# Optimization experiments

Hardware: AMD Instinct MI355X
Metric: run time of the kernel (lower is better)

## Reference

```python
import jax, jax.numpy as jnp
import numpy as np
from jax import lax

B, C, H, W = 4, 256, 64, 64
NH, DK, DV = 8, 32, 32
KER, PAD = 3, 1


def conv1x1(x, w, b=None):
    # x: [B,C,H,W], w: [O,C] (1x1 conv kernel), b: [O] or None
    y = jnp.einsum('bchw,oc->bohw', x, w)
    if b is not None:
        y = y + b[None, :, None, None]
    return y


def unfold(x, k, pad):
    # F.unfold equivalent: [B,C,H,W] -> [B, C*k*k, H, W] (channel-major patch order)
    return lax.conv_general_dilated_patches(x, (k, k), (1, 1), [(pad, pad), (pad, pad)])


def local_attention(q, k, v, kernel, pad, n_head):
    # per-head local windowed attention over a kernel x kernel neighborhood
    b, c, h, w = q.shape
    d = c // n_head
    kk = kernel * kernel
    qh = q.reshape(b, n_head, d, h, w)
    kpat = unfold(k, kernel, pad).reshape(b, n_head, d, kk, h, w)
    vpat = unfold(v, kernel, pad).reshape(b, n_head, d, kk, h, w)
    scale = 1.0 / np.sqrt(float(d)).astype(np.float32)
    logits = jnp.einsum('bhdxy,bhdkxy->bhkxy', qh, kpat) * scale
    attn = jax.nn.softmax(logits, axis=2)
    out = jnp.einsum('bhkxy,bhdkxy->bhdxy', attn, vpat)
    return out.reshape(b, c, h, w)


def layernorm2d(x, g, b, eps=1e-6):
    mu = jnp.mean(x, axis=1, keepdims=True)
    var = jnp.mean((x - mu) ** 2, axis=1, keepdims=True)
    return (x - mu) / jnp.sqrt(var + eps) * g[None, :, None, None] + b[None, :, None, None]


def batchnorm2d(x, g, b, eps=1e-5):
    mu = jnp.mean(x, axis=(0, 2, 3), keepdims=True)
    var = jnp.mean((x - mu) ** 2, axis=(0, 2, 3), keepdims=True)
    return (x - mu) / jnp.sqrt(var + eps) * g[None, :, None, None] + b[None, :, None, None]


def mha(xq, xkv, wq, wk, wv, wfc, g, bias, kernel, pad):
    residual = xq
    q = conv1x1(xq, wq)
    k = conv1x1(xkv, wk)
    v = conv1x1(xkv, wv)
    o = local_attention(q, k, v, kernel, pad, NH)
    o = conv1x1(o, wfc) + residual
    return layernorm2d(o, g, bias)


def ffn(x, w1, b1, w2, b2, g, bias):
    residual = x
    y = conv1x1(jax.nn.relu(conv1x1(x, w1, b1)), w2, b2)
    y = batchnorm2d(y, g, bias)
    return y + residual


def setup_inputs() -> dict:
    key = jax.random.key(0)
    ks = jax.random.split(key, 16)
    s = 0.05
    d = {
        'input1': jax.random.normal(ks[0], (B, C, H, W), jnp.float32),
        'input2': jax.random.normal(ks[1], (B, C, H, W), jnp.float32),
        'slf_wq': jax.random.normal(ks[2], (NH * DK, C), jnp.float32) * s,
        'slf_wk': jax.random.normal(ks[3], (NH * DK, C), jnp.float32) * s,
        'slf_wv': jax.random.normal(ks[4], (NH * DV, C), jnp.float32) * s,
        'slf_fc': jax.random.normal(ks[5], (C, NH * DV), jnp.float32) * s,
        'slf_g': jnp.ones((C,), jnp.float32),
        'slf_b': jnp.zeros((C,), jnp.float32),
        'crs_wq': jax.random.normal(ks[6], (NH * DK, C), jnp.float32) * s,
        'crs_wk': jax.random.normal(ks[7], (NH * DK, C), jnp.float32) * s,
        'crs_wv': jax.random.normal(ks[8], (NH * DV, C), jnp.float32) * s,
        'crs_fc': jax.random.normal(ks[9], (C, NH * DV), jnp.float32) * s,
        'crs_g': jnp.ones((C,), jnp.float32),
        'crs_b': jnp.zeros((C,), jnp.float32),
        'ffn_w1': jax.random.normal(ks[10], (C, C), jnp.float32) * s,
        'ffn_b1': jnp.zeros((C,), jnp.float32),
        'ffn_w2': jax.random.normal(ks[11], (C, C), jnp.float32) * s,
        'ffn_b2': jnp.zeros((C,), jnp.float32),
        'ffn_bn_g': jnp.ones((C,), jnp.float32),
        'ffn_bn_b': jnp.zeros((C,), jnp.float32),
        'kernel': KER,
        'pad': PAD,
    }
    return d


def reference(input1, input2, slf_wq, slf_wk, slf_wv, slf_fc, slf_g, slf_b,
              crs_wq, crs_wk, crs_wv, crs_fc, crs_g, crs_b,
              ffn_w1, ffn_b1, ffn_w2, ffn_b2, ffn_bn_g, ffn_bn_b, kernel, pad):
    slf1 = mha(input1, input1, slf_wq, slf_wk, slf_wv, slf_fc, slf_g, slf_b, kernel, pad)
    slf2 = mha(input2, input2, slf_wq, slf_wk, slf_wv, slf_fc, slf_g, slf_b, kernel, pad)
    crs1 = mha(slf1, slf2, crs_wq, crs_wk, crs_wv, crs_fc, crs_g, crs_b, kernel, pad)
    crs2 = mha(slf2, slf1, crs_wq, crs_wk, crs_wv, crs_fc, crs_g, crs_b, kernel, pad)
    out1 = ffn(crs1, ffn_w1, ffn_b1, ffn_w2, ffn_b2, ffn_bn_g, ffn_bn_b)
    out2 = ffn(crs2, ffn_w1, ffn_b1, ffn_w2, ffn_b2, ffn_bn_g, ffn_bn_b)
    return (out1, out2)
```

## Files before the change

### kernel.cpp

```cpp
#include <hip/hip_runtime.h>
#include <stdint.h>

using u16 = unsigned short;
typedef __bf16 bf16x8 __attribute__((ext_vector_type(8)));
typedef float f32x4 __attribute__((ext_vector_type(4)));

#define NPIX 16384
#define CDIM 256

__device__ __forceinline__ float b2f(u16 u) {
  union { unsigned i; float f; } c; c.i = ((unsigned)u) << 16; return c.f;
}
__device__ __forceinline__ u16 f2b(float x) {
  union { float f; unsigned i; } c; c.f = x;
  unsigned r = c.i + 0x7fffu + ((c.i >> 16) & 1u);
  return (u16)(r >> 16);
}
__device__ __forceinline__ unsigned pack2(float a, float b) {
  return (unsigned)f2b(a) | ((unsigned)f2b(b) << 16);
}
__device__ __forceinline__ void unpack8(uint4 w, float* f) {
  f[0] = b2f((u16)(w.x & 0xffffu)); f[1] = b2f((u16)(w.x >> 16));
  f[2] = b2f((u16)(w.y & 0xffffu)); f[3] = b2f((u16)(w.y >> 16));
  f[4] = b2f((u16)(w.z & 0xffffu)); f[5] = b2f((u16)(w.z >> 16));
  f[6] = b2f((u16)(w.w & 0xffffu)); f[7] = b2f((u16)(w.w >> 16));
}

__device__ __forceinline__ void async16(u16* l, const u16* g) {
  __builtin_amdgcn_global_load_lds((const __attribute__((address_space(1))) void*)g,
                                   (__attribute__((address_space(3))) void*)l, 16, 0, 0);
}

template <int NI>
__device__ __forceinline__ void stage_swz(u16* lds, const u16* src, int tid) {
#pragma unroll
  for (int i = 0; i < NI; ++i) {
    const int idx = i * 256 + tid;
    const int row = idx >> 3;
    const int c8 = (idx & 7) ^ (row & 7);
    async16(lds + idx * 8, src + (size_t)row * 256 + c8 * 8);
  }
}

__global__ void cvt_w(const float* s0, const float* s1, const float* s2,
                      const float* s3, const float* s4, const float* s5,
                      const float* s6, const float* s7, const float* s8,
                      const float* s9, u16* __restrict__ dst,
                      float* __restrict__ stats) {
  if (blockIdx.x == 0 && blockIdx.y == 0) {
    ((float4*)stats)[threadIdx.x] = float4{0.f, 0.f, 0.f, 0.f};
  }
  const int m = blockIdx.y;
  const float* s;
  switch (m) {
    case 0: s = s0; break; case 1: s = s1; break; case 2: s = s2; break;
    case 3: s = s3; break; case 4: s = s4; break; case 5: s = s5; break;
    case 6: s = s6; break; case 7: s = s7; break; case 8: s = s8; break;
    default: s = s9; break;
  }
  const int i = (blockIdx.x * 256 + threadIdx.x) * 4;
  float4 v = *(const float4*)(s + i);
  uint2 o;
  o.x = pack2(v.x, v.y);
  o.y = pack2(v.z, v.w);
  *(uint2*)(dst + (size_t)m * 65536 + i) = o;
}

__global__ void transpose_in(const float* __restrict__ x1, const float* __restrict__ x2,
                             u16* __restrict__ X1, u16* __restrict__ X2) {
  __shared__ u16 tile[64][65];
  const int t = threadIdx.x;
  const int z = blockIdx.z;
  const float* x = (z < 4) ? x1 : x2;
  u16* X = (z < 4) ? X1 : X2;
  const int b = z & 3, c0 = blockIdx.y * 64, hw0 = blockIdx.x * 64;
  {
    const int hw_l = t & 63, cb = t >> 6;
#pragma unroll
    for (int i = 0; i < 16; ++i) {
      const int c_l = cb * 16 + i;
      tile[c_l][hw_l] = f2b(x[((size_t)(b * 256 + c0 + c_l)) * 4096 + hw0 + hw_l]);
    }
  }
  __syncthreads();
  {
    const int c_l = t & 63, hb = t >> 6;
#pragma unroll
    for (int i = 0; i < 16; ++i) {
      const int hw_l = hb * 16 + i;
      X[((size_t)(b * 4096 + hw0 + hw_l)) * 256 + c0 + c_l] = tile[c_l][hw_l];
    }
  }
}

struct P6 { const u16* X[6]; const u16* W[3]; u16* D[6]; };

__global__ void gemm_qkv(P6 a) {
  __shared__ u16 As[128 * 64];
  __shared__ u16 Bs[128 * 64];
  const int tid = threadIdx.x;
  const int wave = tid >> 6, lane = tid & 63;
  const int p0 = blockIdx.x * 128;
  const int g = blockIdx.y >> 1, o0 = (blockIdx.y & 1) * 128;
  const int z = blockIdx.z;
  const u16* X = a.X[z * 3 + g];
  const u16* W = a.W[g];
  u16* D = a.D[z * 3 + g];
  const int wr = wave & 1, wc = wave >> 1;
  const int l15 = lane & 15, l4 = lane >> 4;
  const int sw = l15 & 7;
  f32x4 acc[4][4] = {};

  for (int kt = 0; kt < 4; ++kt) {
    const int k0 = kt * 64;
    stage_swz<4>(As, X + (size_t)p0 * 256 + k0, tid);
    stage_swz<4>(Bs, W + (size_t)o0 * 256 + k0, tid);
    __syncthreads();
#pragma unroll
    for (int kk = 0; kk < 2; ++kk) {
      const int cs = ((kk * 4 + l4) ^ sw) * 8;
      bf16x8 af[4], bfr[4];
#pragma unroll
      for (int mi = 0; mi < 4; ++mi)
        af[mi] = *(const bf16x8*)&As[(wr * 64 + mi * 16 + l15) * 64 + cs];
#pragma unroll
      for (int ni = 0; ni < 4; ++ni)
        bfr[ni] = *(const bf16x8*)&Bs[(wc * 64 + ni * 16 + l15) * 64 + cs];
#pragma unroll
      for (int mi = 0; mi < 4; ++mi)
#pragma unroll
        for (int ni = 0; ni < 4; ++ni)
          acc[mi][ni] = __builtin_amdgcn_mfma_f32_16x16x32_bf16(af[mi], bfr[ni],
                                                                acc[mi][ni], 0, 0, 0);
    }
    __syncthreads();
  }
#pragma unroll
  for (int ni = 0; ni < 4; ++ni) {
    const int o = o0 + wc * 64 + ni * 16 + l15;
#pragma unroll
    for (int mi = 0; mi < 4; ++mi)
#pragma unroll
      for (int r = 0; r < 4; ++r) {
        const int p = p0 + wr * 64 + mi * 16 + l4 * 4 + r;
        D[(size_t)p * 256 + o] = f2b(acc[mi][ni][r]);
      }
  }
}

struct Pfc { const u16* X[2]; const u16* res[2]; u16* dst[2];
             const u16* W; const float* g; const float* b; };

__global__ void gemm_fc_ln(Pfc a) {
  __shared__ u16 As[64 * 64];
  __shared__ u16 Bs[256 * 64];
  __shared__ float red[2][64][4];
  const int tid = threadIdx.x;
  const int wave = tid >> 6, lane = tid & 63;
  const int l15 = lane & 15, l4 = lane >> 4;
  const int sw = l15 & 7;
  const int p0 = blockIdx.x * 64;
  const int z = blockIdx.y;
  const u16* X = a.X[z];
  const u16* res = a.res[z];
  u16* dst = a.dst[z];
  f32x4 acc[4][4] = {};

  for (int kt = 0; kt < 4; ++kt) {
    const int k0 = kt * 64;
    stage_swz<2>(As, X + (size_t)p0 * 256 + k0, tid);
    stage_swz<8>(Bs, a.W + k0, tid);
    __syncthreads();
#pragma unroll
    for (int kk = 0; kk < 2; ++kk) {
      const int cs = ((kk * 4 + l4) ^ sw) * 8;
      bf16x8 af[4], bfr[4];
#pragma unroll
      for (int mi = 0; mi < 4; ++mi)
        af[mi] = *(const bf16x8*)&As[(mi * 16 + l15) * 64 + cs];
#pragma unroll
      for (int ni = 0; ni < 4; ++ni)
        bfr[ni] = *(const bf16x8*)&Bs[(wave * 64 + ni * 16 + l15) * 64 + cs];
#pragma unroll
      for (int mi = 0; mi < 4; ++mi)
#pragma unroll
        for (int ni = 0; ni < 4; ++ni)
          acc[mi][ni] = __builtin_amdgcn_mfma_f32_16x16x32_bf16(af[mi], bfr[ni],
                                                                acc[mi][ni], 0, 0, 0);
    }
    __syncthreads();
  }

#pragma unroll
  for (int mi = 0; mi < 4; ++mi) {
#pragma unroll
    for (int r = 0; r < 4; ++r) {
      const int pl = mi * 16 + l4 * 4 + r;
      const int p = p0 + pl;
      float s = 0.f, s2 = 0.f;
#pragma unroll
      for (int ni = 0; ni < 4; ++ni) {
        const int o = wave * 64 + ni * 16 + l15;
        float vv = acc[mi][ni][r] + b2f(res[(size_t)p * 256 + o]);
        acc[mi][ni][r] = vv;
        s += vv; s2 += vv * vv;
      }
#pragma unroll
      for (int m = 1; m < 16; m <<= 1) {
        s += __shfl_xor(s, m); s2 += __shfl_xor(s2, m);
      }
      if (l15 == 0) { red[0][pl][wave] = s; red[1][pl][wave] = s2; }
    }
  }
  __syncthreads();

  float gv[4], bv[4];
#pragma unroll
  for (int ni = 0; ni < 4; ++ni) {
    const int o = wave * 64 + ni * 16 + l15;
    gv[ni] = a.g[o]; bv[ni] = a.b[o];
  }
#pragma unroll
  for (int mi = 0; mi < 4; ++mi) {
#pragma unroll
    for (int r = 0; r < 4; ++r) {
      const int pl = mi * 16 + l4 * 4 + r;
      const float st = red[0][pl][0] + red[0][pl][1] + red[0][pl][2] + red[0][pl][3];
      const float s2t = red[1][pl][0] + red[1][pl][1] + red[1][pl][2] + red[1][pl][3];
      const float mu = st * (1.f / 256.f);
      const float var = s2t * (1.f / 256.f) - mu * mu;
      const float inv = rsqrtf(var + 1e-6f);
      const int p = p0 + pl;
#pragma unroll
      for (int ni = 0; ni < 4; ++ni) {
        const int o = wave * 64 + ni * 16 + l15;
        dst[(size_t)p * 256 + o] = f2b((acc[mi][ni][r] - mu) * inv * gv[ni] + bv[ni]);
      }
    }
  }
}

struct Pg { const u16* X[2]; u16* Y[2]; float* st[2];
            const u16* W; const float* bias; };

template <int HAS_BIAS, int RELU, int DO_STATS>
__global__ void gemm_kernel(Pg a) {
  __shared__ u16 As[128 * 64];
  __shared__ u16 Bs[64 * 64];
  const int tid = threadIdx.x;
  const int wave = tid >> 6, lane = tid & 63;
  const int p0 = blockIdx.x * 128, o0 = blockIdx.y * 64;
  const int z = blockIdx.z;
  const u16* X = a.X[z];
  u16* Y = a.Y[z];
  float* st = a.st[z];
  const int wr = wave & 1, wc = wave >> 1;
  const int l15 = lane & 15, l4 = lane >> 4;
  const int sw = l15 & 7;
  f32x4 acc[4][2] = {};

  for (int kt = 0; kt < 4; ++kt) {
    const int k0 = kt * 64;
    stage_swz<4>(As, X + (size_t)p0 * 256 + k0, tid);
    stage_swz<2>(Bs, a.W + (size_t)o0 * 256 + k0, tid);
    __syncthreads();
#pragma unroll
    for (int kk = 0; kk < 2; ++kk) {
      const int cs = ((kk * 4 + l4) ^ sw) * 8;
      bf16x8 af[4], bfr[2];
#pragma unroll
      for (int mi = 0; mi < 4; ++mi)
        af[mi] = *(const bf16x8*)&As[(wr * 64 + mi * 16 + l15) * 64 + cs];
#pragma unroll
      for (int ni = 0; ni < 2; ++ni)
        bfr[ni] = *(const bf16x8*)&Bs[(wc * 32 + ni * 16 + l15) * 64 + cs];
#pragma unroll
      for (int mi = 0; mi < 4; ++mi)
#pragma unroll
        for (int ni = 0; ni < 2; ++ni)
          acc[mi][ni] = __builtin_amdgcn_mfma_f32_16x16x32_bf16(af[mi], bfr[ni],
                                                                acc[mi][ni], 0, 0, 0);
    }
    __syncthreads();
  }
#pragma unroll
  for (int ni = 0; ni < 2; ++ni) {
    const int o = o0 + wc * 32 + ni * 16 + l15;
    float bvv = 0.f;
    if (HAS_BIAS) bvv = a.bias[o];
    float s = 0.f, s2 = 0.f;
#pragma unroll
    for (int mi = 0; mi < 4; ++mi) {
#pragma unroll
      for (int r = 0; r < 4; ++r) {
        const int p = p0 + wr * 64 + mi * 16 + l4 * 4 + r;
        float v = acc[mi][ni][r] + bvv;
        if (RELU) v = fmaxf(v, 0.f);
        const u16 hv = f2b(v);
        Y[(size_t)p * 256 + o] = hv;
        if (DO_STATS) { const float vr = b2f(hv); s += vr; s2 += vr * vr; }
      }
    }
    if (DO_STATS) {
      s += __shfl_xor(s, 16); s2 += __shfl_xor(s2, 16);
      s += __shfl_xor(s, 32); s2 += __shfl_xor(s2, 32);
      if (l4 == 0) { atomicAdd(&st[o], s); atomicAdd(&st[256 + o], s2); }
    }
  }
}

struct Pat { const u16* Q[2]; const u16* K[2]; const u16* V[2]; u16* O[2]; };

__global__ void attn_kernel(Pat a) {
  const int s = blockIdx.y;
  const u16* __restrict__ Q = a.Q[s];
  const u16* __restrict__ K = a.K[s];
  const u16* __restrict__ V = a.V[s];
  u16* O = a.O[s];
  const int t = blockIdx.x * 256 + threadIdx.x;
  const int p = t >> 3, h = t & 7;
  const int y = (p >> 6) & 63, x = p & 63;
  const size_t base = (size_t)p * 256 + h * 32;

  float q[32];
  {
    const uint4* qp = (const uint4*)(Q + base);
#pragma unroll
    for (int i = 0; i < 4; ++i) { uint4 w = qp[i]; unpack8(w, q + i * 8); }
  }
  float lg[9];
  float mx = -1e30f;
#pragma unroll
  for (int j = 0; j < 9; ++j) {
    const int dy = j / 3 - 1, dx = j % 3 - 1;
    const int ny = y + dy, nx = x + dx;
    float l = 0.f;
    if ((unsigned)ny < 64u && (unsigned)nx < 64u) {
      const uint4* kp = (const uint4*)(K + base + (ptrdiff_t)(dy * 64 + dx) * 256);
      float acc = 0.f;
#pragma unroll
      for (int i = 0; i < 4; ++i) {
        float kf[8]; unpack8(kp[i], kf);
#pragma unroll
        for (int d = 0; d < 8; ++d) acc += q[i * 8 + d] * kf[d];
      }
      l = acc * 0.17677669529663687f;
    }
    lg[j] = l;
    mx = fmaxf(mx, l);
  }
  float pr[9], den = 0.f;
#pragma unroll
  for (int j = 0; j < 9; ++j) { pr[j] = __expf(lg[j] - mx); den += pr[j]; }
  float out[32];
#pragma unroll
  for (int d = 0; d < 32; ++d) out[d] = 0.f;
#pragma unroll
  for (int j = 0; j < 9; ++j) {
    const int dy = j / 3 - 1, dx = j % 3 - 1;
    const int ny = y + dy, nx = x + dx;
    if ((unsigned)ny < 64u && (unsigned)nx < 64u) {
      const uint4* vp = (const uint4*)(V + base + (ptrdiff_t)(dy * 64 + dx) * 256);
      const float w = pr[j];
#pragma unroll
      for (int i = 0; i < 4; ++i) {
        float vf[8]; unpack8(vp[i], vf);
#pragma unroll
        for (int d = 0; d < 8; ++d) out[i * 8 + d] += w * vf[d];
      }
    }
  }
  const float inv = 1.f / den;
  uint4* op = (uint4*)(O + base);
#pragma unroll
  for (int i = 0; i < 4; ++i) {
    uint4 w;
    w.x = pack2(out[i * 8 + 0] * inv, out[i * 8 + 1] * inv);
    w.y = pack2(out[i * 8 + 2] * inv, out[i * 8 + 3] * inv);
    w.z = pack2(out[i * 8 + 4] * inv, out[i * 8 + 5] * inv);
    w.w = pack2(out[i * 8 + 6] * inv, out[i * 8 + 7] * inv);
    op[i] = w;
  }
}

struct Pbn { const u16* U[2]; const u16* res[2]; const float* st[2];
             float* out[2]; const float* g; const float* b; };

__global__ void bn_apply(Pbn a) {
  __shared__ float tile[64][65];
  const int t = threadIdx.x;
  const int s = blockIdx.z >> 2, b = blockIdx.z & 3;
  const u16* __restrict__ U = a.U[s];
  const u16* __restrict__ res = a.res[s];
  const float* st = a.st[s];
  float* out = a.out[s];
  const int c0 = blockIdx.y * 64, hw0 = blockIdx.x * 64;
  {
    const int c_l = t & 63, hb = t >> 6;
    const int c = c0 + c_l;
    const float mu = st[c] * (1.f / 16384.f);
    const float var = st[256 + c] * (1.f / 16384.f) - mu * mu;
    const float sc = rsqrtf(var + 1e-5f) * a.g[c];
    const float sh = a.b[c] - mu * sc;
#pragma unroll
    for (int i = 0; i < 16; ++i) {
      const int hw_l = hb * 16 + i;
      const size_t p = (size_t)b * 4096 + hw0 + hw_l;
      const float u = b2f(U[p * 256 + c]);
      const float r = b2f(res[p * 256 + c]);
      tile[hw_l][c_l] = u * sc + sh + r;
    }
  }
  __syncthreads();
  {
    const int hw_l = t & 63, cb2 = t >> 6;
#pragma unroll
    for (int i = 0; i < 16; ++i) {
      const int c_l = cb2 * 16 + i;
      out[((size_t)(b * 256 + c0 + c_l)) * 4096 + hw0 + hw_l] = tile[hw_l][c_l];
    }
  }
}

extern "C" void kernel_launch(void* const* d_in, const int* in_sizes, int n_in,
                              void* d_out, int out_size, void* d_ws, size_t ws_size,
                              hipStream_t stream) {
  const float* input1 = (const float*)d_in[0];
  const float* input2 = (const float*)d_in[1];
  const float* slf_wq = (const float*)d_in[2];
  const float* slf_wk = (const float*)d_in[3];
  const float* slf_wv = (const float*)d_in[4];
  const float* slf_fc = (const float*)d_in[5];
  const float* slf_g  = (const float*)d_in[6];
  const float* slf_b  = (const float*)d_in[7];
  const float* crs_wq = (const float*)d_in[8];
  const float* crs_wk = (const float*)d_in[9];
  const float* crs_wv = (const float*)d_in[10];
  const float* crs_fc = (const float*)d_in[11];
  const float* crs_g  = (const float*)d_in[12];
  const float* crs_b  = (const float*)d_in[13];
  const float* ffn_w1 = (const float*)d_in[14];
  const float* ffn_b1 = (const float*)d_in[15];
  const float* ffn_w2 = (const float*)d_in[16];
  const float* ffn_b2 = (const float*)d_in[17];
  const float* bn_g   = (const float*)d_in[18];
  const float* bn_b   = (const float*)d_in[19];

  float* out = (float*)d_out;
  u16* ws = (u16*)d_ws;
  const size_t TS = (size_t)NPIX * CDIM;
  u16* b[10];
  for (int i = 0; i < 10; ++i) b[i] = ws + (size_t)i * TS;
  u16* wb = ws + 10 * TS;
  u16 *Wsq = wb,             *Wsk = wb + 65536,     *Wsv = wb + 2 * 65536,
      *Wsf = wb + 3 * 65536, *Wcq = wb + 4 * 65536, *Wck = wb + 5 * 65536,
      *Wcv = wb + 6 * 65536, *Wcf = wb + 7 * 65536, *W1 = wb + 8 * 65536,
      *W2 = wb + 9 * 65536;
  float* stats = (float*)(wb + 10 * 65536);

  const dim3 tb(256);

  cvt_w<<<dim3(64, 10), tb, 0, stream>>>(slf_wq, slf_wk, slf_wv, slf_fc,
                                         crs_wq, crs_wk, crs_wv, crs_fc,
                                         ffn_w1, ffn_w2, wb, stats);
  transpose_in<<<dim3(64, 4, 8), tb, 0, stream>>>(input1, input2, b[0], b[1]);

  P6 sa;
  sa.X[0] = b[0]; sa.X[1] = b[0]; sa.X[2] = b[0];
  sa.X[3] = b[1]; sa.X[4] = b[1]; sa.X[5] = b[1];
  sa.W[0] = Wsq; sa.W[1] = Wsk; sa.W[2] = Wsv;
  sa.D[0] = b[4]; sa.D[1] = b[5]; sa.D[2] = b[6];
  sa.D[3] = b[7]; sa.D[4] = b[8]; sa.D[5] = b[9];
  gemm_qkv<<<dim3(NPIX / 128, 6, 2), tb, 0, stream>>>(sa);

  Pat aa;
  aa.Q[0] = b[4]; aa.Q[1] = b[7];
  aa.K[0] = b[5]; aa.K[1] = b[8];
  aa.V[0] = b[6]; aa.V[1] = b[9];
  aa.O[0] = b[4]; aa.O[1] = b[7];
  attn_kernel<<<dim3(NPIX * 8 / 256, 2), tb, 0, stream>>>(aa);

  Pfc f1;
  f1.X[0] = b[4]; f1.X[1] = b[7];
  f1.res[0] = b[0]; f1.res[1] = b[1];
  f1.dst[0] = b[2]; f1.dst[1] = b[3];
  f1.W = Wsf; f1.g = slf_g; f1.b = slf_b;
  gemm_fc_ln<<<dim3(NPIX / 64, 2), tb, 0, stream>>>(f1);

  P6 ca;
  ca.X[0] = b[2]; ca.X[1] = b[3]; ca.X[2] = b[3];
  ca.X[3] = b[3]; ca.X[4] = b[2]; ca.X[5] = b[2];
  ca.W[0] = Wcq; ca.W[1] = Wck; ca.W[2] = Wcv;
  ca.D[0] = b[4]; ca.D[1] = b[5]; ca.D[2] = b[6];
  ca.D[3] = b[7]; ca.D[4] = b[8]; ca.D[5] = b[9];
  gemm_qkv<<<dim3(NPIX / 128, 6, 2), tb, 0, stream>>>(ca);
  attn_kernel<<<dim3(NPIX * 8 / 256, 2), tb, 0, stream>>>(aa);

  Pfc f2;
  f2.X[0] = b[4]; f2.X[1] = b[7];
  f2.res[0] = b[2]; f2.res[1] = b[3];
  f2.dst[0] = b[0]; f2.dst[1] = b[1];
  f2.W = Wcf; f2.g = crs_g; f2.b = crs_b;
  gemm_fc_ln<<<dim3(NPIX / 64, 2), tb, 0, stream>>>(f2);

  Pg g1;
  g1.X[0] = b[0]; g1.X[1] = b[1];
  g1.Y[0] = b[4]; g1.Y[1] = b[7];
  g1.st[0] = nullptr; g1.st[1] = nullptr;
  g1.W = W1; g1.bias = ffn_b1;
  gemm_kernel<1, 1, 0><<<dim3(NPIX / 128, CDIM / 64, 2), tb, 0, stream>>>(g1);

  Pg g2;
  g2.X[0] = b[4]; g2.X[1] = b[7];
  g2.Y[0] = b[5]; g2.Y[1] = b[8];
  g2.st[0] = stats; g2.st[1] = stats + 512;
  g2.W = W2; g2.bias = ffn_b2;
  gemm_kernel<1, 0, 1><<<dim3(NPIX / 128, CDIM / 64, 2), tb, 0, stream>>>(g2);

  Pbn bn;
  bn.U[0] = b[5]; bn.U[1] = b[8];
  bn.res[0] = b[0]; bn.res[1] = b[1];
  bn.st[0] = stats; bn.st[1] = stats + 512;
  bn.out[0] = out; bn.out[1] = out + TS;
  bn.g = bn_g; bn.b = bn_b;
  bn_apply<<<dim3(64, 4, 8), tb, 0, stream>>>(bn);
}
```

Measured before the change: 311.5 us.

## Double-buffer GEMM staging, unify GEMM kernels, merge prep kernels, widen fc_ln tiles

```diff
diff --git a/kernel.cpp b/kernel.cpp
--- a/kernel.cpp
+++ b/kernel.cpp
@@ -3,6 +3,7 @@
 
 using u16 = unsigned short;
 typedef __bf16 bf16x8 __attribute__((ext_vector_type(8)));
+typedef __bf16 bf16x2 __attribute__((ext_vector_type(2)));
 typedef float f32x4 __attribute__((ext_vector_type(4)));
 
 #define NPIX 16384
@@ -12,12 +13,10 @@
   union { unsigned i; float f; } c; c.i = ((unsigned)u) << 16; return c.f;
 }
 __device__ __forceinline__ u16 f2b(float x) {
-  union { float f; unsigned i; } c; c.f = x;
-  unsigned r = c.i + 0x7fffu + ((c.i >> 16) & 1u);
-  return (u16)(r >> 16);
+  union { __bf16 h; u16 u; } c; c.h = (__bf16)x; return c.u;
 }
 __device__ __forceinline__ unsigned pack2(float a, float b) {
-  return (unsigned)f2b(a) | ((unsigned)f2b(b) << 16);
+  union { bf16x2 v; unsigned u; } c; c.v[0] = (__bf16)a; c.v[1] = (__bf16)b; return c.u;
 }
 __device__ __forceinline__ void unpack8(uint4 w, float* f) {
   f[0] = b2f((u16)(w.x & 0xffffu)); f[1] = b2f((u16)(w.x >> 16));
@@ -31,49 +30,51 @@
                                    (__attribute__((address_space(3))) void*)l, 16, 0, 0);
 }
 
-template <int NI>
+template <int NI, int NT>
 __device__ __forceinline__ void stage_swz(u16* lds, const u16* src, int tid) {
 #pragma unroll
   for (int i = 0; i < NI; ++i) {
-    const int idx = i * 256 + tid;
+    const int idx = i * NT + tid;
     const int row = idx >> 3;
     const int c8 = (idx & 7) ^ (row & 7);
     async16(lds + idx * 8, src + (size_t)row * 256 + c8 * 8);
   }
 }
 
-__global__ void cvt_w(const float* s0, const float* s1, const float* s2,
-                      const float* s3, const float* s4, const float* s5,
-                      const float* s6, const float* s7, const float* s8,
-                      const float* s9, u16* __restrict__ dst,
-                      float* __restrict__ stats) {
-  if (blockIdx.x == 0 && blockIdx.y == 0) {
-    ((float4*)stats)[threadIdx.x] = float4{0.f, 0.f, 0.f, 0.f};
-  }
-  const int m = blockIdx.y;
-  const float* s;
-  switch (m) {
-    case 0: s = s0; break; case 1: s = s1; break; case 2: s = s2; break;
-    case 3: s = s3; break; case 4: s = s4; break; case 5: s = s5; break;
-    case 6: s = s6; break; case 7: s = s7; break; case 8: s = s8; break;
-    default: s = s9; break;
-  }
-  const int i = (blockIdx.x * 256 + threadIdx.x) * 4;
-  float4 v = *(const float4*)(s + i);
-  uint2 o;
-  o.x = pack2(v.x, v.y);
-  o.y = pack2(v.z, v.w);
-  *(uint2*)(dst + (size_t)m * 65536 + i) = o;
-}
-
-__global__ void transpose_in(const float* __restrict__ x1, const float* __restrict__ x2,
-                             u16* __restrict__ X1, u16* __restrict__ X2) {
+__global__ void prep(const float* __restrict__ x1, const float* __restrict__ x2,
+                     u16* __restrict__ X1, u16* __restrict__ X2,
+                     const float* s0, const float* s1, const float* s2,
+                     const float* s3, const float* s4, const float* s5,
+                     const float* s6, const float* s7, const float* s8,
+                     const float* s9, u16* __restrict__ wdst,
+                     float* __restrict__ stats) {
+  const int t = threadIdx.x;
+  const int yy = blockIdx.y;
+  if (yy >= 32) {
+    const int m = yy - 32;
+    if (m == 0 && blockIdx.x == 0) {
+      ((float4*)stats)[t] = float4{0.f, 0.f, 0.f, 0.f};
+    }
+    const float* s;
+    switch (m) {
+      case 0: s = s0; break; case 1: s = s1; break; case 2: s = s2; break;
+      case 3: s = s3; break; case 4: s = s4; break; case 5: s = s5; break;
+      case 6: s = s6; break; case 7: s = s7; break; case 8: s = s8; break;
+      default: s = s9; break;
+    }
+    const int i = (blockIdx.x * 256 + t) * 4;
+    float4 v = *(const float4*)(s + i);
+    uint2 o;
+    o.x = pack2(v.x, v.y);
+    o.y = pack2(v.z, v.w);
+    *(uint2*)(wdst + (size_t)m * 65536 + i) = o;
+    return;
+  }
   __shared__ u16 tile[64][65];
-  const int t = threadIdx.x;
-  const int z = blockIdx.z;
+  const int z = yy >> 2;
   const float* x = (z < 4) ? x1 : x2;
   u16* X = (z < 4) ? X1 : X2;
-  const int b = z & 3, c0 = blockIdx.y * 64, hw0 = blockIdx.x * 64;
+  const int b = z & 3, c0 = (yy & 3) * 64, hw0 = blockIdx.x * 64;
   {
     const int hw_l = t & 63, cb = t >> 6;
 #pragma unroll
@@ -93,39 +94,51 @@
   }
 }
 
-struct P6 { const u16* X[6]; const u16* W[3]; u16* D[6]; };
-
-__global__ void gemm_qkv(P6 a) {
-  __shared__ u16 As[128 * 64];
-  __shared__ u16 Bs[128 * 64];
+struct PG { const u16* X[6]; const u16* W[3]; u16* D[6];
+            const float* bias; float* st[2]; };
+
+template <int NG, int HAS_BIAS, int RELU, int DO_STATS>
+__global__ void gemm128(PG a) {
+  __shared__ u16 As[2][8192];
+  __shared__ u16 Bs[2][8192];
   const int tid = threadIdx.x;
   const int wave = tid >> 6, lane = tid & 63;
   const int p0 = blockIdx.x * 128;
-  const int g = blockIdx.y >> 1, o0 = (blockIdx.y & 1) * 128;
+  const int g = (NG == 3) ? (blockIdx.y >> 1) : 0;
+  const int o0 = (NG == 3) ? ((blockIdx.y & 1) * 128) : (blockIdx.y * 128);
   const int z = blockIdx.z;
-  const u16* X = a.X[z * 3 + g];
+  const u16* X = a.X[z * NG + g];
   const u16* W = a.W[g];
-  u16* D = a.D[z * 3 + g];
+  u16* D = a.D[z * NG + g];
   const int wr = wave & 1, wc = wave >> 1;
   const int l15 = lane & 15, l4 = lane >> 4;
   const int sw = l15 & 7;
   f32x4 acc[4][4] = {};
 
+  const u16* Xp = X + (size_t)p0 * 256;
+  const u16* Wp = W + (size_t)o0 * 256;
+  stage_swz<4, 256>(As[0], Xp, tid);
+  stage_swz<4, 256>(Bs[0], Wp, tid);
+  __syncthreads();
+
   for (int kt = 0; kt < 4; ++kt) {
-    const int k0 = kt * 64;
-    stage_swz<4>(As, X + (size_t)p0 * 256 + k0, tid);
-    stage_swz<4>(Bs, W + (size_t)o0 * 256 + k0, tid);
-    __syncthreads();
+    const int cur = kt & 1;
+    if (kt < 3) {
+      stage_swz<4, 256>(As[cur ^ 1], Xp + (kt + 1) * 64, tid);
+      stage_swz<4, 256>(Bs[cur ^ 1], Wp + (kt + 1) * 64, tid);
+    }
+    const u16* ab = As[cur];
+    const u16* bb = Bs[cur];
 #pragma unroll
     for (int kk = 0; kk < 2; ++kk) {
       const int cs = ((kk * 4 + l4) ^ sw) * 8;
       bf16x8 af[4], bfr[4];
 #pragma unroll
       for (int mi = 0; mi < 4; ++mi)
-        af[mi] = *(const bf16x8*)&As[(wr * 64 + mi * 16 + l15) * 64 + cs];
+        af[mi] = *(const bf16x8*)&ab[(wr * 64 + mi * 16 + l15) * 64 + cs];
 #pragma unroll
       for (int ni = 0; ni < 4; ++ni)
-        bfr[ni] = *(const bf16x8*)&Bs[(wc * 64 + ni * 16 + l15) * 64 + cs];
+        bfr[ni] = *(const bf16x8*)&bb[(wc * 64 + ni * 16 + l15) * 64 + cs];
 #pragma unroll
       for (int mi = 0; mi < 4; ++mi)
 #pragma unroll
@@ -135,52 +148,78 @@
     }
     __syncthreads();
   }
+
 #pragma unroll
   for (int ni = 0; ni < 4; ++ni) {
     const int o = o0 + wc * 64 + ni * 16 + l15;
-#pragma unroll
-    for (int mi = 0; mi < 4; ++mi)
+    float bvv = 0.f;
+    if (HAS_BIAS) bvv = a.bias[o];
+    float s = 0.f, s2 = 0.f;
+#pragma unroll
+    for (int mi = 0; mi < 4; ++mi) {
 #pragma unroll
       for (int r = 0; r < 4; ++r) {
         const int p = p0 + wr * 64 + mi * 16 + l4 * 4 + r;
-        D[(size_t)p * 256 + o] = f2b(acc[mi][ni][r]);
-      }
+        float v = acc[mi][ni][r] + bvv;
+        if (RELU) v = fmaxf(v, 0.f);
+        const u16 hv = f2b(v);
+        D[(size_t)p * 256 + o] = hv;
+        if (DO_STATS) { const float vr = b2f(hv); s += vr; s2 += vr * vr; }
+      }
+    }
+    if (DO_STATS) {
+      s += __shfl_xor(s, 16); s2 += __shfl_xor(s2, 16);
+      s += __shfl_xor(s, 32); s2 += __shfl_xor(s2, 32);
+      if (l4 == 0) {
+        atomicAdd(&a.st[z][o], s);
+        atomicAdd(&a.st[z][256 + o], s2);
+      }
+    }
   }
 }
 
 struct Pfc { const u16* X[2]; const u16* res[2]; u16* dst[2];
              const u16* W; const float* g; const float* b; };
 
-__global__ void gemm_fc_ln(Pfc a) {
-  __shared__ u16 As[64 * 64];
-  __shared__ u16 Bs[256 * 64];
-  __shared__ float red[2][64][4];
+__global__ __launch_bounds__(512) void gemm_fc_ln(Pfc a) {
+  __shared__ u16 As[2][8192];
+  __shared__ u16 Bs[2][16384];
+  __shared__ float red[2][128][4];
   const int tid = threadIdx.x;
   const int wave = tid >> 6, lane = tid & 63;
+  const int wr = wave & 1, wc = wave >> 1;
   const int l15 = lane & 15, l4 = lane >> 4;
   const int sw = l15 & 7;
-  const int p0 = blockIdx.x * 64;
+  const int p0 = blockIdx.x * 128;
   const int z = blockIdx.y;
   const u16* X = a.X[z];
   const u16* res = a.res[z];
   u16* dst = a.dst[z];
   f32x4 acc[4][4] = {};
 
+  const u16* Xp = X + (size_t)p0 * 256;
+  stage_swz<2, 512>(As[0], Xp, tid);
+  stage_swz<4, 512>(Bs[0], a.W, tid);
+  __syncthreads();
+
   for (int kt = 0; kt < 4; ++kt) {
-    const int k0 = kt * 64;
-    stage_swz<2>(As, X + (size_t)p0 * 256 + k0, tid);
-    stage_swz<8>(Bs, a.W + k0, tid);
-    __syncthreads();
+    const int cur = kt & 1;
+    if (kt < 3) {
+      stage_swz<2, 512>(As[cur ^ 1], Xp + (kt + 1) * 64, tid);
+      stage_swz<4, 512>(Bs[cur ^ 1], a.W + (kt + 1) * 64, tid);
+    }
+    const u16* ab = As[cur];
+    const u16* bb = Bs[cur];
 #pragma unroll
     for (int kk = 0; kk < 2; ++kk) {
       const int cs = ((kk * 4 + l4) ^ sw) * 8;
       bf16x8 af[4], bfr[4];
 #pragma unroll
       for (int mi = 0; mi < 4; ++mi)
-        af[mi] = *(const bf16x8*)&As[(mi * 16 + l15) * 64 + cs];
+        af[mi] = *(const bf16x8*)&ab[(wr * 64 + mi * 16 + l15) * 64 + cs];
 #pragma unroll
       for (int ni = 0; ni < 4; ++ni)
-        bfr[ni] = *(const bf16x8*)&Bs[(wave * 64 + ni * 16 + l15) * 64 + cs];
+        bfr[ni] = *(const bf16x8*)&bb[(wc * 64 + ni * 16 + l15) * 64 + cs];
 #pragma unroll
       for (int mi = 0; mi < 4; ++mi)
 #pragma unroll
@@ -195,12 +234,12 @@
   for (int mi = 0; mi < 4; ++mi) {
 #pragma unroll
     for (int r = 0; r < 4; ++r) {
-      const int pl = mi * 16 + l4 * 4 + r;
+      const int pl = wr * 64 + mi * 16 + l4 * 4 + r;
       const int p = p0 + pl;
       float s = 0.f, s2 = 0.f;
 #pragma unroll
       for (int ni = 0; ni < 4; ++ni) {
-        const int o = wave * 64 + ni * 16 + l15;
+        const int o = wc * 64 + ni * 16 + l15;
         float vv = acc[mi][ni][r] + b2f(res[(size_t)p * 256 + o]);
         acc[mi][ni][r] = vv;
         s += vv; s2 += vv * vv;
@@ -209,7 +248,7 @@
       for (int m = 1; m < 16; m <<= 1) {
         s += __shfl_xor(s, m); s2 += __shfl_xor(s2, m);
       }
-      if (l15 == 0) { red[0][pl][wave] = s; red[1][pl][wave] = s2; }
+      if (l15 == 0) { red[0][pl][wc] = s; red[1][pl][wc] = s2; }
     }
   }
   __syncthreads();
@@ -217,14 +256,14 @@
   float gv[4], bv[4];
 #pragma unroll
   for (int ni = 0; ni < 4; ++ni) {
-    const int o = wave * 64 + ni * 16 + l15;
+    const int o = wc * 64 + ni * 16 + l15;
     gv[ni] = a.g[o]; bv[ni] = a.b[o];
   }
 #pragma unroll
   for (int mi = 0; mi < 4; ++mi) {
 #pragma unroll
     for (int r = 0; r < 4; ++r) {
-      const int pl = mi * 16 + l4 * 4 + r;
+      const int pl = wr * 64 + mi * 16 + l4 * 4 + r;
       const float st = red[0][pl][0] + red[0][pl][1] + red[0][pl][2] + red[0][pl][3];
       const float s2t = red[1][pl][0] + red[1][pl][1] + red[1][pl][2] + red[1][pl][3];
       const float mu = st * (1.f / 256.f);
@@ -233,78 +272,9 @@
       const int p = p0 + pl;
 #pragma unroll
       for (int ni = 0; ni < 4; ++ni) {
-        const int o = wave * 64 + ni * 16 + l15;
+        const int o = wc * 64 + ni * 16 + l15;
         dst[(size_t)p * 256 + o] = f2b((acc[mi][ni][r] - mu) * inv * gv[ni] + bv[ni]);
       }
-    }
-  }
-}
-
-struct Pg { const u16* X[2]; u16* Y[2]; float* st[2];
-            const u16* W; const float* bias; };
-
-template <int HAS_BIAS, int RELU, int DO_STATS>
-__global__ void gemm_kernel(Pg a) {
-  __shared__ u16 As[128 * 64];
-  __shared__ u16 Bs[64 * 64];
-  const int tid = threadIdx.x;
-  const int wave = tid >> 6, lane = tid & 63;
-  const int p0 = blockIdx.x * 128, o0 = blockIdx.y * 64;
-  const int z = blockIdx.z;
-  const u16* X = a.X[z];
-  u16* Y = a.Y[z];
-  float* st = a.st[z];
-  const int wr = wave & 1, wc = wave >> 1;
-  const int l15 = lane & 15, l4 = lane >> 4;
-  const int sw = l15 & 7;
-  f32x4 acc[4][2] = {};
-
-  for (int kt = 0; kt < 4; ++kt) {
-    const int k0 = kt * 64;
-    stage_swz<4>(As, X + (size_t)p0 * 256 + k0, tid);
-    stage_swz<2>(Bs, a.W + (size_t)o0 * 256 + k0, tid);
-    __syncthreads();
-#pragma unroll
-    for (int kk = 0; kk < 2; ++kk) {
-      const int cs = ((kk * 4 + l4) ^ sw) * 8;
-      bf16x8 af[4], bfr[2];
-#pragma unroll
-      for (int mi = 0; mi < 4; ++mi)
-        af[mi] = *(const bf16x8*)&As[(wr * 64 + mi * 16 + l15) * 64 + cs];
-#pragma unroll
-      for (int ni = 0; ni < 2; ++ni)
-        bfr[ni] = *(const bf16x8*)&Bs[(wc * 32 + ni * 16 + l15) * 64 + cs];
-#pragma unroll
-      for (int mi = 0; mi < 4; ++mi)
-#pragma unroll
-        for (int ni = 0; ni < 2; ++ni)
-          acc[mi][ni] = __builtin_amdgcn_mfma_f32_16x16x32_bf16(af[mi], bfr[ni],
-                                                                acc[mi][ni], 0, 0, 0);
-    }
-    __syncthreads();
-  }
-#pragma unroll
-  for (int ni = 0; ni < 2; ++ni) {
-    const int o = o0 + wc * 32 + ni * 16 + l15;
-    float bvv = 0.f;
-    if (HAS_BIAS) bvv = a.bias[o];
-    float s = 0.f, s2 = 0.f;
-#pragma unroll
-    for (int mi = 0; mi < 4; ++mi) {
-#pragma unroll
-      for (int r = 0; r < 4; ++r) {
-        const int p = p0 + wr * 64 + mi * 16 + l4 * 4 + r;
-        float v = acc[mi][ni][r] + bvv;
-        if (RELU) v = fmaxf(v, 0.f);
-        const u16 hv = f2b(v);
-        Y[(size_t)p * 256 + o] = hv;
-        if (DO_STATS) { const float vr = b2f(hv); s += vr; s2 += vr * vr; }
-      }
-    }
-    if (DO_STATS) {
-      s += __shfl_xor(s, 16); s2 += __shfl_xor(s2, 16);
-      s += __shfl_xor(s, 32); s2 += __shfl_xor(s2, 32);
-      if (l4 == 0) { atomicAdd(&st[o], s); atomicAdd(&st[256 + o], s2); }
     }
   }
 }
@@ -460,18 +430,19 @@
 
   const dim3 tb(256);
 
-  cvt_w<<<dim3(64, 10), tb, 0, stream>>>(slf_wq, slf_wk, slf_wv, slf_fc,
-                                         crs_wq, crs_wk, crs_wv, crs_fc,
-                                         ffn_w1, ffn_w2, wb, stats);
-  transpose_in<<<dim3(64, 4, 8), tb, 0, stream>>>(input1, input2, b[0], b[1]);
-
-  P6 sa;
+  prep<<<dim3(64, 42), tb, 0, stream>>>(input1, input2, b[0], b[1],
+                                        slf_wq, slf_wk, slf_wv, slf_fc,
+                                        crs_wq, crs_wk, crs_wv, crs_fc,
+                                        ffn_w1, ffn_w2, wb, stats);
+
+  PG sa;
   sa.X[0] = b[0]; sa.X[1] = b[0]; sa.X[2] = b[0];
   sa.X[3] = b[1]; sa.X[4] = b[1]; sa.X[5] = b[1];
   sa.W[0] = Wsq; sa.W[1] = Wsk; sa.W[2] = Wsv;
   sa.D[0] = b[4]; sa.D[1] = b[5]; sa.D[2] = b[6];
   sa.D[3] = b[7]; sa.D[4] = b[8]; sa.D[5] = b[9];
-  gemm_qkv<<<dim3(NPIX / 128, 6, 2), tb, 0, stream>>>(sa);
+  sa.bias = nullptr; sa.st[0] = nullptr; sa.st[1] = nullptr;
+  gemm128<3, 0, 0, 0><<<dim3(NPIX / 128, 6, 2), tb, 0, stream>>>(sa);
 
   Pat aa;
   aa.Q[0] = b[4]; aa.Q[1] = b[7];
@@ -485,15 +456,16 @@
   f1.res[0] = b[0]; f1.res[1] = b[1];
   f1.dst[0] = b[2]; f1.dst[1] = b[3];
   f1.W = Wsf; f1.g = slf_g; f1.b = slf_b;
-  gemm_fc_ln<<<dim3(NPIX / 64, 2), tb, 0, stream>>>(f1);
-
-  P6 ca;
+  gemm_fc_ln<<<dim3(NPIX / 128, 2), dim3(512), 0, stream>>>(f1);
+
+  PG ca;
   ca.X[0] = b[2]; ca.X[1] = b[3]; ca.X[2] = b[3];
   ca.X[3] = b[3]; ca.X[4] = b[2]; ca.X[5] = b[2];
   ca.W[0] = Wcq; ca.W[1] = Wck; ca.W[2] = Wcv;
   ca.D[0] = b[4]; ca.D[1] = b[5]; ca.D[2] = b[6];
   ca.D[3] = b[7]; ca.D[4] = b[8]; ca.D[5] = b[9];
-  gemm_qkv<<<dim3(NPIX / 128, 6, 2), tb, 0, stream>>>(ca);
+  ca.bias = nullptr; ca.st[0] = nullptr; ca.st[1] = nullptr;
+  gemm128<3, 0, 0, 0><<<dim3(NPIX / 128, 6, 2), tb, 0, stream>>>(ca);
   attn_kernel<<<dim3(NPIX * 8 / 256, 2), tb, 0, stream>>>(aa);
 
   Pfc f2;
@@ -501,21 +473,21 @@
   f2.res[0] = b[2]; f2.res[1] = b[3];
   f2.dst[0] = b[0]; f2.dst[1] = b[1];
   f2.W = Wcf; f2.g = crs_g; f2.b = crs_b;
-  gemm_fc_ln<<<dim3(NPIX / 64, 2), tb, 0, stream>>>(f2);
-
-  Pg g1;
+  gemm_fc_ln<<<dim3(NPIX / 128, 2), dim3(512), 0, stream>>>(f2);
+
+  PG g1;
   g1.X[0] = b[0]; g1.X[1] = b[1];
-  g1.Y[0] = b[4]; g1.Y[1] = b[7];
-  g1.st[0] = nullptr; g1.st[1] = nullptr;
-  g1.W = W1; g1.bias = ffn_b1;
-  gemm_kernel<1, 1, 0><<<dim3(NPIX / 128, CDIM / 64, 2), tb, 0, stream>>>(g1);
-
-  Pg g2;
+  g1.W[0] = W1;
+  g1.D[0] = b[4]; g1.D[1] = b[7];
+  g1.bias = ffn_b1; g1.st[0] = nullptr; g1.st[1] = nullptr;
+  gemm128<1, 1, 1, 0><<<dim3(NPIX / 128, 2, 2), tb, 0, stream>>>(g1);
+
+  PG g2;
   g2.X[0] = b[4]; g2.X[1] = b[7];
-  g2.Y[0] = b[5]; g2.Y[1] = b[8];
-  g2.st[0] = stats; g2.st[1] = stats + 512;
-  g2.W = W2; g2.bias = ffn_b2;
-  gemm_kernel<1, 0, 1><<<dim3(NPIX / 128, CDIM / 64, 2), tb, 0, stream>>>(g2);
+  g2.W[0] = W2;
+  g2.D[0] = b[5]; g2.D[1] = b[8];
+  g2.bias = ffn_b2; g2.st[0] = stats; g2.st[1] = stats + 512;
+  gemm128<1, 1, 0, 1><<<dim3(NPIX / 128, 2, 2), tb, 0, stream>>>(g2);
 
   Pbn bn;
   bn.U[0] = b[5]; bn.U[1] = b[8];
```

New measurement: 301.6 us. 1.03x faster.
